# Performance work log

Hardware: AMD Instinct MI355X
Metric: run time of the kernel (lower is better)

## Reference

```python
import jax, jax.numpy as jnp
import numpy as np

B, F, N, NO = 1, 512, 8192, 21
L1, L2, L3 = 640, 256, 128


def setup_inputs() -> dict:
    key = jax.random.key(0)
    ks = jax.random.split(key, 32)
    rn = lambda k, s: jax.random.normal(k, s, dtype=jnp.float32)
    inp = {
        "emb1": rn(ks[0], (B, F, N)),
        "emb2": rn(ks[1], (B, F, N)),
        "t1": rn(ks[2], (B, 3, N)),
        "t2": rn(ks[3], (B, 3, N)),
        "obj": jax.random.randint(ks[4], (B, 1), 0, NO, dtype=jnp.int32),
    }
    # 1x1 Conv1d weights == dense (out,in) matrices + bias
    dims_r = [(L1, 2 * F), (L2, L1), (L3, L2), (NO * 4, L3)]
    dims_t = [(L1, 2 * F), (L2, L1), (L3, L2), (NO * 3, L3)]
    ki = 5
    for br, dims in (("r", dims_r), ("t", dims_t)):
        for i, (o, c) in enumerate(dims, start=1):
            inp[f"w{i}{br}"] = rn(ks[ki], (o, c)) * (1.0 / np.sqrt(c)); ki += 1
            inp[f"b{i}{br}"] = rn(ks[ki], (o,)) * 0.01; ki += 1
    return inp


def _knn1(ref, qry):
    # ref, qry: (3, N). For each query point j, index of nearest ref point.
    g = ref.T @ qry  # (N_ref, N_qry)
    d2 = jnp.sum(ref * ref, axis=0)[:, None] + jnp.sum(qry * qry, axis=0)[None, :] - 2.0 * g
    return jnp.argmin(d2, axis=0)  # (N_qry,)


def _branch(x, w1, b1, w2, b2, w3, b3, w4, b4):
    h = jax.nn.relu(w1 @ x + b1[:, None])
    h = jax.nn.relu(w2 @ h + b2[:, None])
    h = jax.nn.relu(w3 @ h + b3[:, None])
    return w4 @ h + b4[:, None]


def reference(emb1, emb2, t1, t2, obj,
              w1r, b1r, w2r, b2r, w3r, b3r, w4r, b4r,
              w1t, b1t, w2t, b2t, w3t, b3t, w4t, b4t):
    bs, num_feat, num_points = emb1.shape
    t1 = t1.reshape(bs, 3, -1)
    t2 = t2.reshape(bs, 3, -1)
    # brute-force 1-NN of each t2 point among t1 points (bs == 1)
    idx = _knn1(t1[0], t2[0])  # (N,) zero-based (torch code subtracts 1 from 1-based inds)
    emb1g = emb1[0][:, idx]  # gather matched features, (F, N)
    # torch.stack([emb1,emb2],dim=1).view(bs, 2F, N) == channel concat [emb1g; emb2]
    emb = jnp.concatenate([emb1g, emb2[0]], axis=0)  # (2F, N)
    rx = _branch(emb, w1r, b1r, w2r, b2r, w3r, b3r, w4r, b4r).reshape(NO, 4, num_points)
    tx = _branch(emb, w1t, b1t, w2t, b2t, w3t, b3t, w4t, b4t).reshape(NO, 3, num_points)
    obj0 = obj[0]  # (1,)
    out_rx = jnp.transpose(rx[obj0], (0, 2, 1))  # (1, N, 4)
    out_tx = jnp.transpose(tx[obj0], (0, 2, 1))  # (1, N, 3)
    return out_rx, out_tx
```

## Files before the change

### kernel.cpp

```cpp
#include <hip/hip_runtime.h>

typedef unsigned short u16;
typedef unsigned long long u64;
typedef __bf16 bf16x8 __attribute__((ext_vector_type(8)));
typedef float f32x4 __attribute__((ext_vector_type(4)));

__device__ __forceinline__ float b2f(u16 v) {
    return __uint_as_float(((unsigned int)v) << 16);
}
__device__ __forceinline__ u16 f2b(float f) {
    unsigned int u = __float_as_uint(f);
    u += 0x7fffu + ((u >> 16) & 1u);
    return (u16)(u >> 16);
}

__device__ __forceinline__ void ld_lds16(const u16* g, u16* l) {
    __builtin_amdgcn_global_load_lds(
        (__attribute__((address_space(1))) void*)(uintptr_t)(const void*)g,
        (__attribute__((address_space(3))) void*)l, 16, 0, 0);
}

#define PREP_PACK_END  832
#define PREP_KNN_END   1344
#define PREP_TRANS_END 3392

__global__ __launch_bounds__(256) void prep_k(
    const float* __restrict__ w1r, const float* __restrict__ w1t,
    const float* __restrict__ w2r, const float* __restrict__ w2t,
    const float* __restrict__ w3r, const float* __restrict__ w3t,
    u16* __restrict__ wdst,
    const float* __restrict__ t1, const float* __restrict__ t2,
    u64* __restrict__ part,
    const float* __restrict__ e1, const float* __restrict__ e2,
    u16* __restrict__ o1, u16* __restrict__ o2)
{
    __shared__ __align__(16) float smem[64 * 65];
    const int bid = blockIdx.x;
    const int t = threadIdx.x;

    if (bid < PREP_PACK_END) {
        size_t i = (size_t)bid * 2048 + (size_t)t * 8;
        const float* src; size_t off;
        if (i < 655360)       { src = w1r; off = 0; }
        else if (i < 1310720) { src = w1t; off = 655360; }
        else if (i < 1474560) { src = w2r; off = 1310720; }
        else if (i < 1638400) { src = w2t; off = 1474560; }
        else if (i < 1671168) { src = w3r; off = 1638400; }
        else                  { src = w3t; off = 1671168; }
        const float4 lo = *(const float4*)(src + (i - off));
        const float4 hi = *(const float4*)(src + (i - off) + 4);
        ushort4 o0v, o1v;
        o0v.x = f2b(lo.x); o0v.y = f2b(lo.y); o0v.z = f2b(lo.z); o0v.w = f2b(lo.w);
        o1v.x = f2b(hi.x); o1v.y = f2b(hi.y); o1v.z = f2b(hi.z); o1v.w = f2b(hi.w);
        *(ushort4*)(wdst + i) = o0v;
        *(ushort4*)(wdst + i + 4) = o1v;
    } else if (bid < PREP_KNN_END) {
        float4* ref = (float4*)smem;
        const int rb = bid - PREP_PACK_END;
        const int rs = rb & 63;
        const int qb = rb >> 6;
        if (t < 128) {
            int i = rs * 128 + t;
            float x = t1[i], y = t1[8192 + i], z = t1[16384 + i];
            float rr = __fadd_rn(__fadd_rn(__fmul_rn(x, x), __fmul_rn(y, y)), __fmul_rn(z, z));
            ref[t] = make_float4(x, y, z, rr);
        }
        __syncthreads();

        float qx[4], qy[4], qz[4], qq[4], bestd[4];
        int besti[4];
        const int q0 = qb * 1024 + t;
#pragma unroll
        for (int j = 0; j < 4; ++j) {
            int q = q0 + j * 256;
            qx[j] = t2[q]; qy[j] = t2[8192 + q]; qz[j] = t2[16384 + q];
            qq[j] = __fadd_rn(__fadd_rn(__fmul_rn(qx[j], qx[j]), __fmul_rn(qy[j], qy[j])),
                              __fmul_rn(qz[j], qz[j]));
            bestd[j] = __uint_as_float(0x7f800000u);
            besti[j] = 0;
        }
        for (int i = 0; i < 128; ++i) {
            float4 r = ref[i];
#pragma unroll
            for (int j = 0; j < 4; ++j) {
                float g = __fmaf_rn(qz[j], r.z, __fmaf_rn(qy[j], r.y, __fmul_rn(qx[j], r.x)));
                float d2 = __fsub_rn(__fadd_rn(r.w, qq[j]), __fmul_rn(2.0f, g));
                if (d2 < bestd[j]) { bestd[j] = d2; besti[j] = i + rs * 128; }
            }
        }
#pragma unroll
        for (int j = 0; j < 4; ++j) {
            u64 key = ((u64)__float_as_uint(bestd[j]) << 32) | (unsigned int)besti[j];
            part[(size_t)rs * 8192 + q0 + j * 256] = key;
        }
    } else {
        float (*tile)[65] = (float(*)[65])smem;
        const int tb = bid - PREP_KNN_END;
        const int z = tb >> 10;
        const int rem = tb & 1023;
        const int fy = rem >> 7;
        const int nx = rem & 127;
        const float* in = z ? e2 : e1;
        u16* out = z ? o2 : o1;
        const int n0 = nx * 64, f0 = fy * 64;
        const int c = t & 63, r4 = t >> 6;
#pragma unroll
        for (int p = 0; p < 16; ++p) {
            int fr = p * 4 + r4;
            tile[fr][c] = in[(size_t)(f0 + fr) * 8192 + n0 + c];
        }
        __syncthreads();
        const int fc = (t & 15) * 4;
        const int nr4 = t >> 4;
#pragma unroll
        for (int p = 0; p < 4; ++p) {
            int nr = p * 16 + nr4;
            ushort4 o;
            o.x = f2b(tile[fc + 0][nr]); o.y = f2b(tile[fc + 1][nr]);
            o.z = f2b(tile[fc + 2][nr]); o.w = f2b(tile[fc + 3][nr]);
            *(ushort4*)&out[(size_t)(n0 + nr) * 512 + f0 + fc] = o;
        }
    }
}

__global__ __launch_bounds__(256) void gemm1_k(
    const u16* __restrict__ Ar, const u16* __restrict__ At,
    const float* __restrict__ biasr, const float* __restrict__ biast,
    const u16* __restrict__ emb1t, const u16* __restrict__ emb2t,
    const u64* __restrict__ part,
    u16* __restrict__ Ct)
{
    constexpr int K = 1024;
    __shared__ __align__(16) u16 lds_a[2 * 128 * 32];
    __shared__ __align__(16) u16 lds_b[2 * 128 * 32];
    __shared__ u64 red[2][128];
    __shared__ unsigned int idx_l[128];

    const int t = threadIdx.x;
    const int n0 = blockIdx.x * 128;
    const int m0 = blockIdx.y * 128;
    const int branch = blockIdx.z;

    const u16* A = branch ? At : Ar;
    const float* bias = branch ? biast : biasr;
    const int out_off = branch * 640;

    const int w = t >> 6, l = t & 63;
    const int sr = l >> 2, sc = (l & 3) * 8;

    {
        const int rrow = t & 127, rhalf = t >> 7;
        const u64* pp = part + (size_t)rhalf * 32 * 8192 + (n0 + rrow);
        u64 best = ~0ull;
#pragma unroll 8
        for (int s = 0; s < 32; ++s) {
            u64 k = pp[(size_t)s * 8192];
            best = k < best ? k : best;
        }
        red[rhalf][rrow] = best;
    }
    __syncthreads();
    if (t < 128) {
        u64 a = red[0][t], b = red[1][t];
        idx_l[t] = (unsigned int)(a < b ? a : b);
    }
    __syncthreads();

    const u16* gA0 = A + (size_t)(m0 + w * 32 + sr) * K + sc;
    const u16* gA1 = gA0 + (size_t)16 * K;
    u16* lA = &lds_a[w * 1024];

    const int row0 = n0 + w * 32 + sr;
    const int row1 = row0 + 16;
    const unsigned int i0 = idx_l[w * 32 + sr];
    const unsigned int i1 = idx_l[w * 32 + sr + 16];
    const u16* gB0 = emb1t + (size_t)i0 * 512 + sc;
    const u16* gB1 = emb1t + (size_t)i1 * 512 + sc;
    u16* lB = &lds_b[w * 1024];

    const int wm = (w & 1) * 64;
    const int wn = (w >> 1) * 64;
    const int lrow = l & 15, quad = l >> 4;
    const u16* fa = &lds_a[(wm + lrow) * 32 + quad * 8];
    const u16* fb = &lds_b[(wn + lrow) * 32 + quad * 8];

    f32x4 acc[4][4];
#pragma unroll
    for (int i = 0; i < 4; ++i)
#pragma unroll
        for (int j = 0; j < 4; ++j)
            acc[i][j] = (f32x4){0.f, 0.f, 0.f, 0.f};

    ld_lds16(gA0,      lA);
    ld_lds16(gA1,      lA + 512);
    ld_lds16(gA0 + 32, lA + 4096);
    ld_lds16(gA1 + 32, lA + 4096 + 512);
    ld_lds16(gB0,      lB);
    ld_lds16(gB1,      lB + 512);
    ld_lds16(gB0 + 32, lB + 4096);
    ld_lds16(gB1 + 32, lB + 4096 + 512);

    for (int kt = 0; kt < K; kt += 64) {
        __syncthreads();
        bf16x8 af[2][4], bfr[2][4];
#pragma unroll
        for (int p = 0; p < 2; ++p)
#pragma unroll
            for (int i = 0; i < 4; ++i) {
                af[p][i]  = *(const bf16x8*)(fa + p * 4096 + i * 16 * 32);
                bfr[p][i] = *(const bf16x8*)(fb + p * 4096 + i * 16 * 32);
            }
        __syncthreads();
        if (kt + 64 < K) {
            gA0 += 64; gA1 += 64;
            if (kt + 64 == 512) {
                gB0 = emb2t + (size_t)row0 * 512 + sc;
                gB1 = emb2t + (size_t)row1 * 512 + sc;
            } else {
                gB0 += 64; gB1 += 64;
            }
            ld_lds16(gA0,      lA);
            ld_lds16(gA1,      lA + 512);
            ld_lds16(gA0 + 32, lA + 4096);
            ld_lds16(gA1 + 32, lA + 4096 + 512);
            ld_lds16(gB0,      lB);
            ld_lds16(gB1,      lB + 512);
            ld_lds16(gB0 + 32, lB + 4096);
            ld_lds16(gB1 + 32, lB + 4096 + 512);
        }
#pragma unroll
        for (int p = 0; p < 2; ++p)
#pragma unroll
            for (int i = 0; i < 4; ++i)
#pragma unroll
                for (int j = 0; j < 4; ++j)
                    acc[i][j] = __builtin_amdgcn_mfma_f32_16x16x32_bf16(
                        af[p][i], bfr[p][j], acc[i][j], 0, 0, 0);
    }

#pragma unroll
    for (int i = 0; i < 4; ++i) {
        const int mbase = m0 + wm + i * 16 + quad * 4;
        const float4 bbv = *(const float4*)&bias[mbase];
#pragma unroll
        for (int j = 0; j < 4; ++j) {
            const int n = n0 + wn + j * 16 + lrow;
            f32x4 v = acc[i][j];
            float x0 = fmaxf(v[0] + bbv.x, 0.f);
            float x1 = fmaxf(v[1] + bbv.y, 0.f);
            float x2 = fmaxf(v[2] + bbv.z, 0.f);
            float x3 = fmaxf(v[3] + bbv.w, 0.f);
            ushort4 o;
            o.x = f2b(x0); o.y = f2b(x1); o.z = f2b(x2); o.w = f2b(x3);
            *(ushort4*)&Ct[(size_t)n * 1280 + out_off + mbase] = o;
        }
    }
}

template <int TN>
__global__ __launch_bounds__(256) void gemm_bt(
    const u16* __restrict__ Ar, const u16* __restrict__ At,
    const float* __restrict__ biasr, const float* __restrict__ biast,
    const u16* __restrict__ Bt, u16* __restrict__ Ct,
    int Mh, int K, int bstride, int b_step, int ostride, int relu)
{
    constexpr int NJ = TN / 32;
    __shared__ __align__(16) u16 lds_a[128 * 32];
    __shared__ __align__(16) u16 lds_b[TN * 32];

    const int t = threadIdx.x;
    const int n0 = blockIdx.x * TN;
    const int m0 = blockIdx.y * 128;
    const int branch = blockIdx.z;

    const u16* A = branch ? At : Ar;
    const float* bias = branch ? biast : biasr;
    const int b_off = branch * b_step;
    const int out_off = branch * Mh;

    const int w = t >> 6, l = t & 63;
    const int sr = l >> 2, sc = (l & 3) * 8;

    const u16* gA0 = A + (size_t)(m0 + w * 32 + sr) * K + sc;
    const u16* gA1 = gA0 + (size_t)16 * K;
    u16* lA0 = &lds_a[w * 1024];
    u16* lA1 = lA0 + 512;

    const u16* gB0;
    const u16* gB1 = nullptr;
    u16 *lB0, *lB1 = nullptr;
    if (TN == 128) {
        gB0 = Bt + (size_t)(n0 + w * 32 + sr) * bstride + b_off + sc;
        gB1 = gB0 + (size_t)16 * bstride;
        lB0 = &lds_b[w * 1024];
        lB1 = lB0 + 512;
    } else {
        gB0 = Bt + (size_t)(n0 + w * 16 + sr) * bstride + b_off + sc;
        lB0 = &lds_b[w * 512];
    }

    const int wm = (w & 1) * 64;
    const int wn = (w >> 1) * (TN / 2);
    const int lrow = l & 15, quad = l >> 4;
    const u16* fa = &lds_a[(wm + lrow) * 32 + quad * 8];
    const u16* fb = &lds_b[(wn + lrow) * 32 + quad * 8];

    f32x4 acc[4][NJ];
#pragma unroll
    for (int i = 0; i < 4; ++i)
#pragma unroll
        for (int j = 0; j < NJ; ++j)
            acc[i][j] = (f32x4){0.f, 0.f, 0.f, 0.f};

    ld_lds16(gA0, lA0); ld_lds16(gA1, lA1);
    ld_lds16(gB0, lB0);
    if (TN == 128) ld_lds16(gB1, lB1);

    for (int kt = 0; kt < K; kt += 32) {
        __syncthreads();
        bf16x8 af[4], bfr[NJ];
#pragma unroll
        for (int i = 0; i < 4; ++i) af[i] = *(const bf16x8*)(fa + i * 16 * 32);
#pragma unroll
        for (int j = 0; j < NJ; ++j) bfr[j] = *(const bf16x8*)(fb + j * 16 * 32);
        __syncthreads();
        if (kt + 32 < K) {
            gA0 += 32; gA1 += 32; gB0 += 32;
            ld_lds16(gA0, lA0); ld_lds16(gA1, lA1);
            ld_lds16(gB0, lB0);
            if (TN == 128) { gB1 += 32; ld_lds16(gB1, lB1); }
        }
#pragma unroll
        for (int i = 0; i < 4; ++i)
#pragma unroll
            for (int j = 0; j < NJ; ++j)
                acc[i][j] = __builtin_amdgcn_mfma_f32_16x16x32_bf16(
                    af[i], bfr[j], acc[i][j], 0, 0, 0);
    }

#pragma unroll
    for (int i = 0; i < 4; ++i) {
        const int mbase = m0 + wm + i * 16 + quad * 4;
        const float4 bbv = *(const float4*)&bias[mbase];
#pragma unroll
        for (int j = 0; j < NJ; ++j) {
            const int n = n0 + wn + j * 16 + lrow;
            f32x4 v = acc[i][j];
            float x0 = v[0] + bbv.x, x1 = v[1] + bbv.y;
            float x2 = v[2] + bbv.z, x3 = v[3] + bbv.w;
            if (relu) {
                x0 = fmaxf(x0, 0.f); x1 = fmaxf(x1, 0.f);
                x2 = fmaxf(x2, 0.f); x3 = fmaxf(x3, 0.f);
            }
            ushort4 o;
            o.x = f2b(x0); o.y = f2b(x1); o.z = f2b(x2); o.w = f2b(x3);
            *(ushort4*)&Ct[(size_t)n * ostride + out_off + mbase] = o;
        }
    }
}

__global__ __launch_bounds__(256) void gemm3_final_k(
    const u16* __restrict__ Ar, const u16* __restrict__ At,
    const float* __restrict__ b3r, const float* __restrict__ b3t,
    const u16* __restrict__ Bt,
    const float* __restrict__ w4r, const float* __restrict__ b4r,
    const float* __restrict__ w4t, const float* __restrict__ b4t,
    const int* __restrict__ objp, float* __restrict__ out)
{
    __shared__ __align__(16) u16 lds_a[128 * 32];
    __shared__ __align__(16) u16 lds_b[64 * 32];
    __shared__ __align__(16) float lds_h[64 * 132];
    __shared__ __align__(16) float lds_w[4 * 132];

    const int t = threadIdx.x;
    const int n0 = blockIdx.x * 64;
    const int branch = blockIdx.y;

    const u16* A = branch ? At : Ar;
    const float* bias = branch ? b3t : b3r;
    const int b_off = branch * 256;

    const int w = t >> 6, l = t & 63;
    const int sr = l >> 2, sc = (l & 3) * 8;

    const u16* gA0 = A + (size_t)(w * 32 + sr) * 256 + sc;
    const u16* gA1 = gA0 + (size_t)16 * 256;
    u16* lA0 = &lds_a[w * 1024];
    u16* lA1 = lA0 + 512;

    const u16* gB0 = Bt + (size_t)(n0 + w * 16 + sr) * 512 + b_off + sc;
    u16* lB0 = &lds_b[w * 512];

    const int wm = (w & 1) * 64;
    const int wn = (w >> 1) * 32;
    const int lrow = l & 15, quad = l >> 4;
    const u16* fa = &lds_a[(wm + lrow) * 32 + quad * 8];
    const u16* fb = &lds_b[(wn + lrow) * 32 + quad * 8];

    f32x4 acc[4][2];
#pragma unroll
    for (int i = 0; i < 4; ++i)
#pragma unroll
        for (int j = 0; j < 2; ++j)
            acc[i][j] = (f32x4){0.f, 0.f, 0.f, 0.f};

    ld_lds16(gA0, lA0); ld_lds16(gA1, lA1);
    ld_lds16(gB0, lB0);

    for (int kt = 0; kt < 256; kt += 32) {
        __syncthreads();
        bf16x8 af[4], bfr[2];
#pragma unroll
        for (int i = 0; i < 4; ++i) af[i] = *(const bf16x8*)(fa + i * 16 * 32);
#pragma unroll
        for (int j = 0; j < 2; ++j) bfr[j] = *(const bf16x8*)(fb + j * 16 * 32);
        __syncthreads();
        if (kt + 32 < 256) {
            gA0 += 32; gA1 += 32; gB0 += 32;
            ld_lds16(gA0, lA0); ld_lds16(gA1, lA1);
            ld_lds16(gB0, lB0);
        }
#pragma unroll
        for (int i = 0; i < 4; ++i)
#pragma unroll
            for (int j = 0; j < 2; ++j)
                acc[i][j] = __builtin_amdgcn_mfma_f32_16x16x32_bf16(
                    af[i], bfr[j], acc[i][j], 0, 0, 0);
    }

#pragma unroll
    for (int i = 0; i < 4; ++i) {
        const int mbase = wm + i * 16 + quad * 4;
        const float4 bbv = *(const float4*)&bias[mbase];
#pragma unroll
        for (int j = 0; j < 2; ++j) {
            const int nl = wn + j * 16 + lrow;
            f32x4 v = acc[i][j];
            float4 x;
            x.x = fmaxf(v[0] + bbv.x, 0.f); x.y = fmaxf(v[1] + bbv.y, 0.f);
            x.z = fmaxf(v[2] + bbv.z, 0.f); x.w = fmaxf(v[3] + bbv.w, 0.f);
            *(float4*)&lds_h[nl * 132 + mbase] = x;
        }
    }
    const int o = objp[0];
    const int NR = branch ? 3 : 4;
    const float* w4 = branch ? w4t : w4r;
    if (t < 128) {
        for (int r = 0; r < NR; ++r)
            lds_w[r * 132 + t] = w4[(size_t)(o * NR + r) * 128 + t];
    }
    __syncthreads();

    const int nl = t >> 2, k = t & 3;
    if (k < NR) {
        const float4* hp = (const float4*)&lds_h[nl * 132];
        const float4* wp4 = (const float4*)&lds_w[k * 132];
        float s = 0.f;
#pragma unroll
        for (int m4 = 0; m4 < 32; ++m4) {
            float4 h = hp[m4], ww = wp4[m4];
            s = fmaf(h.x, ww.x, s); s = fmaf(h.y, ww.y, s);
            s = fmaf(h.z, ww.z, s); s = fmaf(h.w, ww.w, s);
        }
        const int n = n0 + nl;
        if (branch == 0) out[(size_t)n * 4 + k] = s + b4r[o * 4 + k];
        else             out[32768 + (size_t)n * 3 + k] = s + b4t[o * 3 + k];
    }
}

extern "C" void kernel_launch(void* const* d_in, const int* in_sizes, int n_in,
                              void* d_out, int out_size, void* d_ws, size_t ws_size,
                              hipStream_t stream)
{
    const float* emb1 = (const float*)d_in[0];
    const float* emb2 = (const float*)d_in[1];
    const float* t1   = (const float*)d_in[2];
    const float* t2   = (const float*)d_in[3];
    const int*   obj  = (const int*)d_in[4];
    const float* w1r = (const float*)d_in[5];  const float* b1r = (const float*)d_in[6];
    const float* w2r = (const float*)d_in[7];  const float* b2r = (const float*)d_in[8];
    const float* w3r = (const float*)d_in[9];  const float* b3r = (const float*)d_in[10];
    const float* w4r = (const float*)d_in[11]; const float* b4r = (const float*)d_in[12];
    const float* w1t = (const float*)d_in[13]; const float* b1t = (const float*)d_in[14];
    const float* w2t = (const float*)d_in[15]; const float* b2t = (const float*)d_in[16];
    const float* w3t = (const float*)d_in[17]; const float* b3t = (const float*)d_in[18];
    const float* w4t = (const float*)d_in[19]; const float* b4t = (const float*)d_in[20];

    char* ws = (char*)d_ws;
    u64* part  = (u64*)(ws + (1u << 16));
    u16* emb1t = (u16*)(ws + (8u << 20));
    u16* emb2t = (u16*)(ws + (16u << 20));
    u16* h1t   = (u16*)(ws + (24u << 20));
    u16* wp    = (u16*)(ws + (44u << 20));
    u16* h2t   = emb1t;

    u16* w1rp = wp;            u16* w1tp = wp + 655360;
    u16* w2rp = wp + 1310720;  u16* w2tp = wp + 1474560;
    u16* w3rp = wp + 1638400;  u16* w3tp = wp + 1671168;

    prep_k<<<PREP_TRANS_END, 256, 0, stream>>>(w1r, w1t, w2r, w2t, w3r, w3t, wp,
                                               t1, t2, part,
                                               emb1, emb2, emb1t, emb2t);
    gemm1_k<<<dim3(64, 5, 2), 256, 0, stream>>>(w1rp, w1tp, b1r, b1t,
                                                emb1t, emb2t, part, h1t);
    gemm_bt<64><<<dim3(128, 2, 2), 256, 0, stream>>>(w2rp, w2tp, b2r, b2t, h1t, h2t,
                                                     256, 640, 1280, 640, 512, 1);
    gemm3_final_k<<<dim3(128, 2), 256, 0, stream>>>(w3rp, w3tp, b3r, b3t, h2t,
                                                    w4r, b4r, w4t, b4t, obj, (float*)d_out);
}
```

Before: 188.2 us.

## Fuse layer-2/3/4 GEMMs into one kernel and double-buffer gemm1 LDS

Replaces the separate layer-2 GEMM and layer-3+final kernels with one fused kernel. For each 32-point tile it computes h2 in LDS for both branches and then layer 3 and the selected layer-4 outputs, so the h2 round trip through global memory and one launch go away. gemm1 switches from a 64-wide K step with two syncs to a 32-wide double-buffered pipeline with one sync per step. The cost is that the fused kernel launches only 256 blocks, each running both branches serially, with a larger LDS footprint, so occupancy and parallelism drop.

```diff
diff --git a/kernel.cpp b/kernel.cpp
--- a/kernel.cpp
+++ b/kernel.cpp
@@ -5,9 +5,6 @@
 typedef __bf16 bf16x8 __attribute__((ext_vector_type(8)));
 typedef float f32x4 __attribute__((ext_vector_type(4)));
 
-__device__ __forceinline__ float b2f(u16 v) {
-    return __uint_as_float(((unsigned int)v) << 16);
-}
 __device__ __forceinline__ u16 f2b(float f) {
     unsigned int u = __float_as_uint(f);
     u += 0x7fffu + ((u >> 16) & 1u);
@@ -131,8 +128,8 @@
     u16* __restrict__ Ct)
 {
     constexpr int K = 1024;
-    __shared__ __align__(16) u16 lds_a[2 * 128 * 32];
-    __shared__ __align__(16) u16 lds_b[2 * 128 * 32];
+    __shared__ __align__(16) u16 lds_a[2][4096];
+    __shared__ __align__(16) u16 lds_b[2][4096];
     __shared__ u64 red[2][128];
     __shared__ unsigned int idx_l[128];
 
@@ -168,21 +165,14 @@
 
     const u16* gA0 = A + (size_t)(m0 + w * 32 + sr) * K + sc;
     const u16* gA1 = gA0 + (size_t)16 * K;
-    u16* lA = &lds_a[w * 1024];
-
     const int row0 = n0 + w * 32 + sr;
     const int row1 = row0 + 16;
-    const unsigned int i0 = idx_l[w * 32 + sr];
-    const unsigned int i1 = idx_l[w * 32 + sr + 16];
-    const u16* gB0 = emb1t + (size_t)i0 * 512 + sc;
-    const u16* gB1 = emb1t + (size_t)i1 * 512 + sc;
-    u16* lB = &lds_b[w * 1024];
+    const u16* gB0 = emb1t + (size_t)idx_l[w * 32 + sr] * 512 + sc;
+    const u16* gB1 = emb1t + (size_t)idx_l[w * 32 + sr + 16] * 512 + sc;
 
     const int wm = (w & 1) * 64;
     const int wn = (w >> 1) * 64;
     const int lrow = l & 15, quad = l >> 4;
-    const u16* fa = &lds_a[(wm + lrow) * 32 + quad * 8];
-    const u16* fb = &lds_b[(wn + lrow) * 32 + quad * 8];
 
     f32x4 acc[4][4];
 #pragma unroll
@@ -191,51 +181,40 @@
         for (int j = 0; j < 4; ++j)
             acc[i][j] = (f32x4){0.f, 0.f, 0.f, 0.f};
 
-    ld_lds16(gA0,      lA);
-    ld_lds16(gA1,      lA + 512);
-    ld_lds16(gA0 + 32, lA + 4096);
-    ld_lds16(gA1 + 32, lA + 4096 + 512);
-    ld_lds16(gB0,      lB);
-    ld_lds16(gB1,      lB + 512);
-    ld_lds16(gB0 + 32, lB + 4096);
-    ld_lds16(gB1 + 32, lB + 4096 + 512);
-
-    for (int kt = 0; kt < K; kt += 64) {
-        __syncthreads();
-        bf16x8 af[2][4], bfr[2][4];
-#pragma unroll
-        for (int p = 0; p < 2; ++p)
-#pragma unroll
-            for (int i = 0; i < 4; ++i) {
-                af[p][i]  = *(const bf16x8*)(fa + p * 4096 + i * 16 * 32);
-                bfr[p][i] = *(const bf16x8*)(fb + p * 4096 + i * 16 * 32);
-            }
-        __syncthreads();
-        if (kt + 64 < K) {
-            gA0 += 64; gA1 += 64;
-            if (kt + 64 == 512) {
+    ld_lds16(gA0, &lds_a[0][w * 1024]); ld_lds16(gA1, &lds_a[0][w * 1024 + 512]);
+    ld_lds16(gB0, &lds_b[0][w * 1024]); ld_lds16(gB1, &lds_b[0][w * 1024 + 512]);
+    __syncthreads();
+
+    int cur = 0;
+    for (int kt = 0; kt < K; kt += 32) {
+        if (kt + 32 < K) {
+            gA0 += 32; gA1 += 32;
+            if (kt + 32 == 512) {
                 gB0 = emb2t + (size_t)row0 * 512 + sc;
                 gB1 = emb2t + (size_t)row1 * 512 + sc;
             } else {
-                gB0 += 64; gB1 += 64;
-            }
-            ld_lds16(gA0,      lA);
-            ld_lds16(gA1,      lA + 512);
-            ld_lds16(gA0 + 32, lA + 4096);
-            ld_lds16(gA1 + 32, lA + 4096 + 512);
-            ld_lds16(gB0,      lB);
-            ld_lds16(gB1,      lB + 512);
-            ld_lds16(gB0 + 32, lB + 4096);
-            ld_lds16(gB1 + 32, lB + 4096 + 512);
-        }
-#pragma unroll
-        for (int p = 0; p < 2; ++p)
-#pragma unroll
-            for (int i = 0; i < 4; ++i)
-#pragma unroll
-                for (int j = 0; j < 4; ++j)
-                    acc[i][j] = __builtin_amdgcn_mfma_f32_16x16x32_bf16(
-                        af[p][i], bfr[p][j], acc[i][j], 0, 0, 0);
+                gB0 += 32; gB1 += 32;
+            }
+            const int nx = cur ^ 1;
+            ld_lds16(gA0, &lds_a[nx][w * 1024]); ld_lds16(gA1, &lds_a[nx][w * 1024 + 512]);
+            ld_lds16(gB0, &lds_b[nx][w * 1024]); ld_lds16(gB1, &lds_b[nx][w * 1024 + 512]);
+        }
+        const u16* fa = &lds_a[cur][(wm + lrow) * 32 + quad * 8];
+        const u16* fb = &lds_b[cur][(wn + lrow) * 32 + quad * 8];
+        bf16x8 af[4], bfr[4];
+#pragma unroll
+        for (int i = 0; i < 4; ++i) {
+            af[i]  = *(const bf16x8*)(fa + i * 512);
+            bfr[i] = *(const bf16x8*)(fb + i * 512);
+        }
+#pragma unroll
+        for (int i = 0; i < 4; ++i)
+#pragma unroll
+            for (int j = 0; j < 4; ++j)
+                acc[i][j] = __builtin_amdgcn_mfma_f32_16x16x32_bf16(
+                    af[i], bfr[j], acc[i][j], 0, 0, 0);
+        __syncthreads();
+        cur ^= 1;
     }
 
 #pragma unroll
@@ -257,214 +236,181 @@
     }
 }
 
-template <int TN>
-__global__ __launch_bounds__(256) void gemm_bt(
-    const u16* __restrict__ Ar, const u16* __restrict__ At,
-    const float* __restrict__ biasr, const float* __restrict__ biast,
-    const u16* __restrict__ Bt, u16* __restrict__ Ct,
-    int Mh, int K, int bstride, int b_step, int ostride, int relu)
-{
-    constexpr int NJ = TN / 32;
-    __shared__ __align__(16) u16 lds_a[128 * 32];
-    __shared__ __align__(16) u16 lds_b[TN * 32];
-
-    const int t = threadIdx.x;
-    const int n0 = blockIdx.x * TN;
-    const int m0 = blockIdx.y * 128;
-    const int branch = blockIdx.z;
-
-    const u16* A = branch ? At : Ar;
-    const float* bias = branch ? biast : biasr;
-    const int b_off = branch * b_step;
-    const int out_off = branch * Mh;
-
-    const int w = t >> 6, l = t & 63;
-    const int sr = l >> 2, sc = (l & 3) * 8;
-
-    const u16* gA0 = A + (size_t)(m0 + w * 32 + sr) * K + sc;
-    const u16* gA1 = gA0 + (size_t)16 * K;
-    u16* lA0 = &lds_a[w * 1024];
-    u16* lA1 = lA0 + 512;
-
-    const u16* gB0;
-    const u16* gB1 = nullptr;
-    u16 *lB0, *lB1 = nullptr;
-    if (TN == 128) {
-        gB0 = Bt + (size_t)(n0 + w * 32 + sr) * bstride + b_off + sc;
-        gB1 = gB0 + (size_t)16 * bstride;
-        lB0 = &lds_b[w * 1024];
-        lB1 = lB0 + 512;
-    } else {
-        gB0 = Bt + (size_t)(n0 + w * 16 + sr) * bstride + b_off + sc;
-        lB0 = &lds_b[w * 512];
-    }
-
-    const int wm = (w & 1) * 64;
-    const int wn = (w >> 1) * (TN / 2);
-    const int lrow = l & 15, quad = l >> 4;
-    const u16* fa = &lds_a[(wm + lrow) * 32 + quad * 8];
-    const u16* fb = &lds_b[(wn + lrow) * 32 + quad * 8];
-
-    f32x4 acc[4][NJ];
-#pragma unroll
-    for (int i = 0; i < 4; ++i)
-#pragma unroll
-        for (int j = 0; j < NJ; ++j)
-            acc[i][j] = (f32x4){0.f, 0.f, 0.f, 0.f};
-
-    ld_lds16(gA0, lA0); ld_lds16(gA1, lA1);
-    ld_lds16(gB0, lB0);
-    if (TN == 128) ld_lds16(gB1, lB1);
-
-    for (int kt = 0; kt < K; kt += 32) {
-        __syncthreads();
-        bf16x8 af[4], bfr[NJ];
-#pragma unroll
-        for (int i = 0; i < 4; ++i) af[i] = *(const bf16x8*)(fa + i * 16 * 32);
-#pragma unroll
-        for (int j = 0; j < NJ; ++j) bfr[j] = *(const bf16x8*)(fb + j * 16 * 32);
-        __syncthreads();
-        if (kt + 32 < K) {
-            gA0 += 32; gA1 += 32; gB0 += 32;
-            ld_lds16(gA0, lA0); ld_lds16(gA1, lA1);
-            ld_lds16(gB0, lB0);
-            if (TN == 128) { gB1 += 32; ld_lds16(gB1, lB1); }
-        }
-#pragma unroll
-        for (int i = 0; i < 4; ++i)
-#pragma unroll
-            for (int j = 0; j < NJ; ++j)
-                acc[i][j] = __builtin_amdgcn_mfma_f32_16x16x32_bf16(
-                    af[i], bfr[j], acc[i][j], 0, 0, 0);
-    }
-
-#pragma unroll
-    for (int i = 0; i < 4; ++i) {
-        const int mbase = m0 + wm + i * 16 + quad * 4;
-        const float4 bbv = *(const float4*)&bias[mbase];
-#pragma unroll
-        for (int j = 0; j < NJ; ++j) {
-            const int n = n0 + wn + j * 16 + lrow;
-            f32x4 v = acc[i][j];
-            float x0 = v[0] + bbv.x, x1 = v[1] + bbv.y;
-            float x2 = v[2] + bbv.z, x3 = v[3] + bbv.w;
-            if (relu) {
-                x0 = fmaxf(x0, 0.f); x1 = fmaxf(x1, 0.f);
-                x2 = fmaxf(x2, 0.f); x3 = fmaxf(x3, 0.f);
-            }
-            ushort4 o;
-            o.x = f2b(x0); o.y = f2b(x1); o.z = f2b(x2); o.w = f2b(x3);
-            *(ushort4*)&Ct[(size_t)n * ostride + out_off + mbase] = o;
-        }
-    }
-}
-
-__global__ __launch_bounds__(256) void gemm3_final_k(
-    const u16* __restrict__ Ar, const u16* __restrict__ At,
+__global__ __launch_bounds__(256) void gemm23_k(
+    const u16* __restrict__ w2rp, const u16* __restrict__ w2tp,
+    const float* __restrict__ b2r, const float* __restrict__ b2t,
+    const u16* __restrict__ w3rp, const u16* __restrict__ w3tp,
     const float* __restrict__ b3r, const float* __restrict__ b3t,
-    const u16* __restrict__ Bt,
+    const u16* __restrict__ h1t,
     const float* __restrict__ w4r, const float* __restrict__ b4r,
     const float* __restrict__ w4t, const float* __restrict__ b4t,
     const int* __restrict__ objp, float* __restrict__ out)
 {
-    __shared__ __align__(16) u16 lds_a[128 * 32];
-    __shared__ __align__(16) u16 lds_b[64 * 32];
-    __shared__ __align__(16) float lds_h[64 * 132];
-    __shared__ __align__(16) float lds_w[4 * 132];
+    __shared__ __align__(16) u16 smem[27680];
+    u16* const lds_a  = smem;
+    u16* const lds_b  = smem + 16384;
+    u16* const h2     = smem + 18432;
+    float* const ldsw = (float*)(smem + 26624);
+    float* const h3buf = (float*)smem;
 
     const int t = threadIdx.x;
-    const int n0 = blockIdx.x * 64;
-    const int branch = blockIdx.y;
-
-    const u16* A = branch ? At : Ar;
-    const float* bias = branch ? b3t : b3r;
-    const int b_off = branch * 256;
-
+    const int n0 = blockIdx.x * 32;
     const int w = t >> 6, l = t & 63;
     const int sr = l >> 2, sc = (l & 3) * 8;
-
-    const u16* gA0 = A + (size_t)(w * 32 + sr) * 256 + sc;
-    const u16* gA1 = gA0 + (size_t)16 * 256;
-    u16* lA0 = &lds_a[w * 1024];
-    u16* lA1 = lA0 + 512;
-
-    const u16* gB0 = Bt + (size_t)(n0 + w * 16 + sr) * 512 + b_off + sc;
-    u16* lB0 = &lds_b[w * 512];
-
-    const int wm = (w & 1) * 64;
-    const int wn = (w >> 1) * 32;
     const int lrow = l & 15, quad = l >> 4;
-    const u16* fa = &lds_a[(wm + lrow) * 32 + quad * 8];
-    const u16* fb = &lds_b[(wn + lrow) * 32 + quad * 8];
-
-    f32x4 acc[4][2];
-#pragma unroll
-    for (int i = 0; i < 4; ++i)
-#pragma unroll
-        for (int j = 0; j < 2; ++j)
-            acc[i][j] = (f32x4){0.f, 0.f, 0.f, 0.f};
-
-    ld_lds16(gA0, lA0); ld_lds16(gA1, lA1);
-    ld_lds16(gB0, lB0);
-
-    for (int kt = 0; kt < 256; kt += 32) {
-        __syncthreads();
-        bf16x8 af[4], bfr[2];
-#pragma unroll
-        for (int i = 0; i < 4; ++i) af[i] = *(const bf16x8*)(fa + i * 16 * 32);
-#pragma unroll
-        for (int j = 0; j < 2; ++j) bfr[j] = *(const bf16x8*)(fb + j * 16 * 32);
-        __syncthreads();
-        if (kt + 32 < 256) {
-            gA0 += 32; gA1 += 32; gB0 += 32;
-            ld_lds16(gA0, lA0); ld_lds16(gA1, lA1);
-            ld_lds16(gB0, lB0);
-        }
+    const int o = objp[0];
+
+    for (int br = 0; br < 2; ++br) {
+        const u16* w2p = br ? w2tp : w2rp;
+        const float* b2 = br ? b2t : b2r;
+        const u16* w3p = br ? w3tp : w3rp;
+        const float* b3 = br ? b3t : b3r;
+        const float* w4 = br ? w4t : w4r;
+        const int NR = br ? 3 : 4;
+
+        const u16* gA0 = w2p + (size_t)(w * 64 +      sr) * 640 + sc;
+        const u16* gA1 = w2p + (size_t)(w * 64 + 16 + sr) * 640 + sc;
+        const u16* gA2 = w2p + (size_t)(w * 64 + 32 + sr) * 640 + sc;
+        const u16* gA3 = w2p + (size_t)(w * 64 + 48 + sr) * 640 + sc;
+        const u16* gB0 = h1t + (size_t)(n0 + w * 16 + sr) * 1280 + br * 640 + sc;
+
+        f32x4 acc2[4][2];
 #pragma unroll
         for (int i = 0; i < 4; ++i)
 #pragma unroll
             for (int j = 0; j < 2; ++j)
-                acc[i][j] = __builtin_amdgcn_mfma_f32_16x16x32_bf16(
-                    af[i], bfr[j], acc[i][j], 0, 0, 0);
-    }
-
-#pragma unroll
-    for (int i = 0; i < 4; ++i) {
-        const int mbase = wm + i * 16 + quad * 4;
-        const float4 bbv = *(const float4*)&bias[mbase];
-#pragma unroll
-        for (int j = 0; j < 2; ++j) {
-            const int nl = wn + j * 16 + lrow;
-            f32x4 v = acc[i][j];
-            float4 x;
-            x.x = fmaxf(v[0] + bbv.x, 0.f); x.y = fmaxf(v[1] + bbv.y, 0.f);
-            x.z = fmaxf(v[2] + bbv.z, 0.f); x.w = fmaxf(v[3] + bbv.w, 0.f);
-            *(float4*)&lds_h[nl * 132 + mbase] = x;
-        }
-    }
-    const int o = objp[0];
-    const int NR = branch ? 3 : 4;
-    const float* w4 = branch ? w4t : w4r;
-    if (t < 128) {
-        for (int r = 0; r < NR; ++r)
-            lds_w[r * 132 + t] = w4[(size_t)(o * NR + r) * 128 + t];
-    }
-    __syncthreads();
-
-    const int nl = t >> 2, k = t & 3;
-    if (k < NR) {
-        const float4* hp = (const float4*)&lds_h[nl * 132];
-        const float4* wp4 = (const float4*)&lds_w[k * 132];
-        float s = 0.f;
-#pragma unroll
-        for (int m4 = 0; m4 < 32; ++m4) {
-            float4 h = hp[m4], ww = wp4[m4];
-            s = fmaf(h.x, ww.x, s); s = fmaf(h.y, ww.y, s);
-            s = fmaf(h.z, ww.z, s); s = fmaf(h.w, ww.w, s);
-        }
-        const int n = n0 + nl;
-        if (branch == 0) out[(size_t)n * 4 + k] = s + b4r[o * 4 + k];
-        else             out[32768 + (size_t)n * 3 + k] = s + b4t[o * 3 + k];
+                acc2[i][j] = (f32x4){0.f, 0.f, 0.f, 0.f};
+
+        {
+            u16* lA = lds_a + w * 2048;
+            ld_lds16(gA0, lA);        ld_lds16(gA1, lA + 512);
+            ld_lds16(gA2, lA + 1024); ld_lds16(gA3, lA + 1536);
+            if (w < 2) ld_lds16(gB0, lds_b + w * 512);
+        }
+        __syncthreads();
+
+        int cur = 0;
+        for (int kt = 0; kt < 640; kt += 32) {
+            if (kt + 32 < 640) {
+                gA0 += 32; gA1 += 32; gA2 += 32; gA3 += 32; gB0 += 32;
+                u16* lA = lds_a + (cur ^ 1) * 8192 + w * 2048;
+                ld_lds16(gA0, lA);        ld_lds16(gA1, lA + 512);
+                ld_lds16(gA2, lA + 1024); ld_lds16(gA3, lA + 1536);
+                if (w < 2) ld_lds16(gB0, lds_b + (cur ^ 1) * 1024 + w * 512);
+            }
+            const u16* fa = lds_a + cur * 8192 + (w * 64 + lrow) * 32 + quad * 8;
+            const u16* fb = lds_b + cur * 1024 + lrow * 32 + quad * 8;
+            bf16x8 af[4], bv[2];
+#pragma unroll
+            for (int i = 0; i < 4; ++i) af[i] = *(const bf16x8*)(fa + i * 512);
+#pragma unroll
+            for (int j = 0; j < 2; ++j) bv[j] = *(const bf16x8*)(fb + j * 512);
+#pragma unroll
+            for (int i = 0; i < 4; ++i)
+#pragma unroll
+                for (int j = 0; j < 2; ++j)
+                    acc2[i][j] = __builtin_amdgcn_mfma_f32_16x16x32_bf16(
+                        af[i], bv[j], acc2[i][j], 0, 0, 0);
+            __syncthreads();
+            cur ^= 1;
+        }
+
+#pragma unroll
+        for (int i = 0; i < 4; ++i) {
+            const int mb = w * 64 + i * 16 + quad * 4;
+            const float4 bbv = *(const float4*)&b2[mb];
+#pragma unroll
+            for (int j = 0; j < 2; ++j) {
+                const int nl = j * 16 + lrow;
+                f32x4 v = acc2[i][j];
+                ushort4 ov;
+                ov.x = f2b(fmaxf(v[0] + bbv.x, 0.f));
+                ov.y = f2b(fmaxf(v[1] + bbv.y, 0.f));
+                ov.z = f2b(fmaxf(v[2] + bbv.z, 0.f));
+                ov.w = f2b(fmaxf(v[3] + bbv.w, 0.f));
+                *(ushort4*)&h2[(mb >> 5) * 1024 + nl * 32 + (mb & 31)] = ov;
+            }
+        }
+        if (t < 128) {
+#pragma unroll
+            for (int r = 0; r < 4; ++r)
+                if (r < NR) ldsw[r * 132 + t] = w4[(size_t)(o * NR + r) * 128 + t];
+        }
+
+        const u16* gW0 = w3p + (size_t)(w * 32 +      sr) * 256 + sc;
+        const u16* gW1 = w3p + (size_t)(w * 32 + 16 + sr) * 256 + sc;
+
+        f32x4 acc3[2][2];
+#pragma unroll
+        for (int i = 0; i < 2; ++i)
+#pragma unroll
+            for (int j = 0; j < 2; ++j)
+                acc3[i][j] = (f32x4){0.f, 0.f, 0.f, 0.f};
+
+        {
+            u16* lA = lds_a + w * 1024;
+            ld_lds16(gW0, lA); ld_lds16(gW1, lA + 512);
+        }
+        __syncthreads();
+
+        cur = 0;
+        for (int kt = 0; kt < 256; kt += 32) {
+            if (kt + 32 < 256) {
+                gW0 += 32; gW1 += 32;
+                u16* lA = lds_a + (cur ^ 1) * 8192 + w * 1024;
+                ld_lds16(gW0, lA); ld_lds16(gW1, lA + 512);
+            }
+            const u16* fa = lds_a + cur * 8192 + (w * 32 + lrow) * 32 + quad * 8;
+            const u16* fb = h2 + (kt >> 5) * 1024 + lrow * 32 + quad * 8;
+            bf16x8 af[2], bv[2];
+            af[0] = *(const bf16x8*)(fa);
+            af[1] = *(const bf16x8*)(fa + 512);
+            bv[0] = *(const bf16x8*)(fb);
+            bv[1] = *(const bf16x8*)(fb + 512);
+#pragma unroll
+            for (int i = 0; i < 2; ++i)
+#pragma unroll
+                for (int j = 0; j < 2; ++j)
+                    acc3[i][j] = __builtin_amdgcn_mfma_f32_16x16x32_bf16(
+                        af[i], bv[j], acc3[i][j], 0, 0, 0);
+            __syncthreads();
+            cur ^= 1;
+        }
+
+#pragma unroll
+        for (int i = 0; i < 2; ++i) {
+            const int mb = w * 32 + i * 16 + quad * 4;
+            const float4 bbv = *(const float4*)&b3[mb];
+#pragma unroll
+            for (int j = 0; j < 2; ++j) {
+                const int nl = j * 16 + lrow;
+                f32x4 v = acc3[i][j];
+                float4 x;
+                x.x = fmaxf(v[0] + bbv.x, 0.f); x.y = fmaxf(v[1] + bbv.y, 0.f);
+                x.z = fmaxf(v[2] + bbv.z, 0.f); x.w = fmaxf(v[3] + bbv.w, 0.f);
+                *(float4*)&h3buf[nl * 132 + mb] = x;
+            }
+        }
+        __syncthreads();
+
+        {
+            const int nl = t >> 2, k = t & 3;
+            if (t < 128 && k < NR) {
+                const float4* hp  = (const float4*)&h3buf[nl * 132];
+                const float4* wp4 = (const float4*)&ldsw[k * 132];
+                float s = 0.f;
+#pragma unroll
+                for (int m4 = 0; m4 < 32; ++m4) {
+                    float4 h = hp[m4], ww = wp4[m4];
+                    s = fmaf(h.x, ww.x, s); s = fmaf(h.y, ww.y, s);
+                    s = fmaf(h.z, ww.z, s); s = fmaf(h.w, ww.w, s);
+                }
+                const int n = n0 + nl;
+                if (br == 0) out[(size_t)n * 4 + k] = s + b4r[o * 4 + k];
+                else         out[32768 + (size_t)n * 3 + k] = s + b4t[o * 3 + k];
+            }
+        }
+        __syncthreads();
     }
 }
 
@@ -492,7 +438,6 @@
     u16* emb2t = (u16*)(ws + (16u << 20));
     u16* h1t   = (u16*)(ws + (24u << 20));
     u16* wp    = (u16*)(ws + (44u << 20));
-    u16* h2t   = emb1t;
 
     u16* w1rp = wp;            u16* w1tp = wp + 655360;
     u16* w2rp = wp + 1310720;  u16* w2tp = wp + 1474560;
@@ -503,8 +448,6 @@
                                                emb1, emb2, emb1t, emb2t);
     gemm1_k<<<dim3(64, 5, 2), 256, 0, stream>>>(w1rp, w1tp, b1r, b1t,
                                                 emb1t, emb2t, part, h1t);
-    gemm_bt<64><<<dim3(128, 2, 2), 256, 0, stream>>>(w2rp, w2tp, b2r, b2t, h1t, h2t,
-                                                     256, 640, 1280, 640, 512, 1);
-    gemm3_final_k<<<dim3(128, 2), 256, 0, stream>>>(w3rp, w3tp, b3r, b3t, h2t,
-                                                    w4r, b4r, w4t, b4t, obj, (float*)d_out);
-}
+    gemm23_k<<<256, 256, 0, stream>>>(w2rp, w2tp, b2r, b2t, w3rp, w3tp, b3r, b3t,
+                                      h1t, w4r, b4r, w4t, b4t, obj, (float*)d_out);
+}
```

Result: no change. 190.6 us (+1.2%).
